# Performance work log

Measured on AMD Instinct MI355X. Metric: run time of the kernel, lower is better.

Reference implementation:

```python
import jax, jax.numpy as jnp
import numpy as np

D_MODEL = 512
H = 8
D_K = D_MODEL // H


def setup_inputs() -> dict:
    key = jax.random.key(0)
    ks = jax.random.split(key, 11)
    B, S = 2, 2048
    scale = 1.0 / np.sqrt(D_MODEL)
    return {
        "q": jax.random.normal(ks[0], (B, S, D_MODEL), jnp.float32),
        "v": jax.random.normal(ks[1], (B, S, D_MODEL), jnp.float32),
        "k": jax.random.normal(ks[2], (B, S, D_MODEL), jnp.float32),
        "w_q": jax.random.normal(ks[3], (D_MODEL, D_MODEL), jnp.float32) * scale,
        "b_q": jnp.zeros((D_MODEL,), jnp.float32),
        "w_k": jax.random.normal(ks[4], (D_MODEL, D_MODEL), jnp.float32) * scale,
        "b_k": jnp.zeros((D_MODEL,), jnp.float32),
        "w_v": jax.random.normal(ks[5], (D_MODEL, D_MODEL), jnp.float32) * scale,
        "b_v": jnp.zeros((D_MODEL,), jnp.float32),
        "w_o": jax.random.normal(ks[6], (D_MODEL, D_MODEL), jnp.float32) * scale,
        "b_o": jnp.zeros((D_MODEL,), jnp.float32),
    }


def reference(q, v, k, w_q, b_q, w_k, b_k, w_v, b_v, w_o, b_o):
    B, S, _ = q.shape
    # projections (nn.Linear: x @ W.T + b)
    query = q @ w_q.T + b_q
    key_t = k @ w_k.T + b_k
    value = v @ w_v.T + b_v
    # split heads: [B, S, H, D_K] -> [B, H, S, D_K]
    query = query.reshape(B, S, H, D_K).transpose(0, 2, 1, 3)
    key_t = key_t.reshape(B, S, H, D_K).transpose(0, 2, 1, 3)
    value = value.reshape(B, S, H, D_K).transpose(0, 2, 1, 3)
    # unfused attention: full [B, H, S, S] score matrix
    scores = jnp.einsum("bhqd,bhkd->bhqk", query, key_t) / jnp.sqrt(
        jnp.asarray(D_K, query.dtype)
    )
    attn = jax.nn.softmax(scores, axis=-1)  # dropout inactive in eval
    x = jnp.einsum("bhqk,bhkd->bhqd", attn, value)
    # merge heads and output projection
    x = x.transpose(0, 2, 1, 3).reshape(B, S, D_MODEL)
    return x @ w_o.T + b_o
```

## Files before the change

kernel.cpp:

```cpp
#include <hip/hip_runtime.h>
#include <hip/hip_bf16.h>


typedef __attribute__((ext_vector_type(8))) short short8;
typedef __attribute__((ext_vector_type(4))) short short4v;
typedef __attribute__((ext_vector_type(4))) float f32x4;
typedef __attribute__((ext_vector_type(4))) unsigned int uint4v;

#define DM 512
#define SEQ 2048
#define NROW 4096
#define LOG2E 1.44269504088896341f
#define MFMA(a, b, c) __builtin_amdgcn_mfma_f32_16x16x32_bf16(a, b, c, 0, 0, 0)
#define FENCE() __asm__ __volatile__("" ::: "memory")

#if __has_builtin(__builtin_amdgcn_exp2f)
#define EXP2(x) __builtin_amdgcn_exp2f(x)
#else
#define EXP2(x) exp2f(x)
#endif

__device__ __forceinline__ float bf_bits2f(short s) {
    unsigned int u = ((unsigned int)(unsigned short)s) << 16;
    return __builtin_bit_cast(float, u);
}
__device__ __forceinline__ short f2bf_r(float f) {
    unsigned int u = __builtin_bit_cast(unsigned int, f) + 0x8000u;
    return (short)(u >> 16);
}
__device__ __forceinline__ unsigned int pack_bf16(float lo, float hi) {
    unsigned int ul = __builtin_bit_cast(unsigned int, lo) + 0x8000u;
    unsigned int uh = __builtin_bit_cast(unsigned int, hi) + 0x8000u;
    return __builtin_amdgcn_perm(uh, ul, 0x07060302u);
}

__device__ __forceinline__ void gload_lds16(const void* src, void* lds_dst) {
    __builtin_amdgcn_global_load_lds(
        (const __attribute__((address_space(1))) unsigned int*)src,
        (__attribute__((address_space(3))) unsigned int*)lds_dst, 16, 0, 0);
}

template <int ROWS, int NW, int SH = 0>
__device__ __forceinline__ void stage_tile(const short* __restrict__ gsrc, size_t gstride,
                                           short* lds, int wave, int lane) {
    constexpr int ISSUES = ROWS * 8 / (64 * NW);
    #pragma unroll
    for (int i = 0; i < ISSUES; i++) {
        const int blk = i * NW + wave;
        const int g = blk * 64 + lane;
        const int row = g >> 3;
        const int cb = (g & 7) ^ ((row >> SH) & 7);
        gload_lds16(gsrc + (size_t)row * gstride + cb * 8, lds + (size_t)blk * 512);
    }
}

__device__ __forceinline__ bool detect_f32(const unsigned int* __restrict__ q, int* cnt_lds) {
    if (threadIdx.x == 0) *cnt_lds = 0;
    __syncthreads();
    int local = 0;
    for (int i = threadIdx.x; i < 1024; i += blockDim.x) {
        unsigned int lo = q[i] & 0x7FFFu;
        if (lo >= 0x3000u && lo < 0x4400u) local++;
    }
    if (local) atomicAdd(cnt_lds, local);
    __syncthreads();
    return *cnt_lds < 512;
}

struct ConvArgs { const void* src[11]; short* dst[11]; int n[11]; int* flag; };
__global__ void convert_all(ConvArgs a) {
    __shared__ int cnt;
    const bool f32m = detect_f32((const unsigned int*)a.src[0], &cnt);
    if (threadIdx.x == 0) *a.flag = f32m ? 1 : 0;
    const int tid = blockIdx.x * 256 + threadIdx.x;
    const int stride = gridDim.x * 256;
    if (f32m) {
        for (int s = 0; s < 11; s++) {
            const float4* sp = (const float4*)a.src[s];
            short4v* dp = (short4v*)a.dst[s];
            const int n4 = a.n[s] >> 2;
            for (int i = tid; i < n4; i += stride) {
                float4 v = sp[i];
                short4v o;
                o[0] = f2bf_r(v.x); o[1] = f2bf_r(v.y);
                o[2] = f2bf_r(v.z); o[3] = f2bf_r(v.w);
                dp[i] = o;
            }
        }
    } else {
        for (int s = 0; s < 11; s++) {
            const short4v* sp = (const short4v*)a.src[s];
            short4v* dp = (short4v*)a.dst[s];
            const int n4 = a.n[s] >> 2;
            for (int i = tid; i < n4; i += stride) dp[i] = sp[i];
        }
    }
}

template <int MT, int NT>
__device__ __forceinline__ void gemm_core(const short* __restrict__ A,
                                          const short* __restrict__ W,
                                          int m0, int n0, short* Alds, short* Blds,
                                          int wave, int lane,
                                          f32x4 (&acc)[MT / 64][NT / 16]) {
    const int rc = lane & 15, quad = lane >> 4;
    const short* Ag = A + (size_t)m0 * DM;
    const short* Bg = W + (size_t)n0 * DM;
    constexpr int ABUF = MT * 64, BBUF = NT * 64;
    constexpr int INFLIGHT = (MT + NT) * 8 / 256;
    constexpr int NITER = DM / 64;

    stage_tile<MT, 4>(Ag, DM, Alds, wave, lane);
    stage_tile<NT, 4>(Bg, DM, Blds, wave, lane);

    for (int i = 0; i < NITER; i++) {
        const int cur = i & 1;
        const short* Ac = Alds + cur * ABUF;
        const short* Bc = Blds + cur * BBUF;
        if (i + 1 < NITER) {
            stage_tile<MT, 4>(Ag + (i + 1) * 64, DM, Alds + (cur ^ 1) * ABUF, wave, lane);
            stage_tile<NT, 4>(Bg + (i + 1) * 64, DM, Blds + (cur ^ 1) * BBUF, wave, lane);
            __builtin_amdgcn_s_waitcnt(0x3F70 | INFLIGHT);
        } else {
            __builtin_amdgcn_s_waitcnt(0x3F70);
        }
        FENCE();
        __builtin_amdgcn_s_barrier();
        FENCE();
        #pragma unroll
        for (int h = 0; h < 2; h++) {
            short8 bf[NT / 16];
            #pragma unroll
            for (int nt = 0; nt < NT / 16; nt++) {
                const int br = nt * 16 + rc;
                bf[nt] = *(const short8*)&Bc[br * 64 + (((quad + 4 * h) ^ (br & 7)) * 8)];
            }
            #pragma unroll
            for (int ms = 0; ms < MT / 64; ms++) {
                const int ar = wave * (MT / 4) + ms * 16 + rc;
                short8 af = *(const short8*)&Ac[ar * 64 + (((quad + 4 * h) ^ (ar & 7)) * 8)];
                #pragma unroll
                for (int nt = 0; nt < NT / 16; nt++)
                    acc[ms][nt] = MFMA(af, bf[nt], acc[ms][nt]);
            }
        }
        FENCE();
        __builtin_amdgcn_s_barrier();
        FENCE();
    }
}

struct QKVArgs {
    const short* A[3]; const short* W[3]; const short* Bi[3];
    short* Cq; short* Ck; short* Cv;
};
__global__ __launch_bounds__(256, 2) void qkv_gemm(QKVArgs args) {
    __shared__ __align__(16) short Alds[2][128 * 64];
    __shared__ __align__(16) short Blds[2][128 * 64];
    const int z = blockIdx.z;
    const int wave = threadIdx.x >> 6, lane = threadIdx.x & 63;
    const int rc = lane & 15, quad = lane >> 4;
    const int m0 = blockIdx.x * 128, n0 = blockIdx.y * 128;

    f32x4 acc[2][8] = {};
    gemm_core<128, 128>(args.A[z], args.W[z], m0, n0, &Alds[0][0], &Blds[0][0], wave, lane, acc);
    const short* bias = args.Bi[z];

    if (z == 2) {
        #pragma unroll
        for (int ms = 0; ms < 2; ms++) {
            const int mw = m0 + wave * 32 + ms * 16;
            const int b = mw >> 11, sb = (mw & 2047) + quad * 4;
            #pragma unroll
            for (int nt = 0; nt < 8; nt++) {
                const int dg = n0 + nt * 16 + rc;
                const int hh = dg >> 6, dd = dg & 63;
                const float bv = bf_bits2f(bias[dg]);
                short4v pk;
                #pragma unroll
                for (int r = 0; r < 4; r++) pk[r] = f2bf_r(acc[ms][nt][r] + bv);
                *(short4v*)(args.Cv + ((size_t)((b * 8 + hh) * 64 + dd)) * SEQ + sb) = pk;
            }
        }
    } else {
        short* C = (z == 0) ? args.Cq : args.Ck;
        const float sc = (z == 0) ? (0.125f * LOG2E) : 1.0f;
        #pragma unroll
        for (int ms = 0; ms < 2; ms++) {
            const int mw = m0 + wave * 32 + ms * 16;
            #pragma unroll
            for (int nt = 0; nt < 8; nt++) {
                const int col = n0 + nt * 16 + rc;
                const float bv = bf_bits2f(bias[col]);
                #pragma unroll
                for (int r = 0; r < 4; r++)
                    C[(size_t)(mw + quad * 4 + r) * DM + col] = f2bf_r((acc[ms][nt][r] + bv) * sc);
            }
        }
    }
}

__global__ __launch_bounds__(256, 4) void out_gemm(
    const short* __restrict__ A, const short* __restrict__ W,
    const short* __restrict__ bias, void* __restrict__ Cout,
    const int* __restrict__ dtf) {
    __shared__ __align__(16) short Alds[2][64 * 64];
    __shared__ __align__(16) short Blds[2][64 * 64];
    const bool f32out = (*dtf != 0);
    const int wave = threadIdx.x >> 6, lane = threadIdx.x & 63;
    const int rc = lane & 15, quad = lane >> 4;
    const int m0 = blockIdx.x * 64, n0 = blockIdx.y * 64;
    f32x4 acc[1][4] = {};
    gemm_core<64, 64>(A, W, m0, n0, &Alds[0][0], &Blds[0][0], wave, lane, acc);
    const int mw = m0 + wave * 16;
    #pragma unroll
    for (int nt = 0; nt < 4; nt++) {
        const int col = n0 + nt * 16 + rc;
        const float bv = bf_bits2f(bias[col]);
        #pragma unroll
        for (int r = 0; r < 4; r++) {
            const size_t idx = (size_t)(mw + quad * 4 + r) * DM + col;
            const float val = acc[0][nt][r] + bv;
            if (f32out) ((float*)Cout)[idx] = val;
            else        ((short*)Cout)[idx] = f2bf_r(val);
        }
    }
}

__global__ __launch_bounds__(512, 4) void attn_kernel(
    const short* __restrict__ Q, const short* __restrict__ K,
    const short* __restrict__ Vt, short* __restrict__ X)
{
    __shared__ __align__(16) short S[2][16384];

    const int wave = threadIdx.x >> 6, lane = threadIdx.x & 63;
    const int rc = lane & 15, quad = lane >> 4;
    const int qh = wave & 1, kh = wave >> 1;
    const int L = blockIdx.x;
    const int bh = (L & 7) * 2 + ((L >> 3) >> 5);
    const int qb = (L >> 3) & 31;
    const size_t baseQK = (size_t)(bh >> 3) * SEQ * DM + (size_t)(bh & 7) * 64;
    const short* Qb = Q + baseQK;
    const short* Kb = K + baseQK;
    const short* Vb = Vt + (size_t)bh * 64 * SEQ;
    const int q0 = qb * 64 + qh * 32;

    short8 qa[2][2];
    #pragma unroll
    for (int ms = 0; ms < 2; ms++)
        #pragma unroll
        for (int h = 0; h < 2; h++)
            qa[ms][h] = *(const short8*)(Qb + (size_t)(q0 + ms * 16 + rc) * DM + h * 32 + quad * 8);

    short8 ones;
    #pragma unroll
    for (int j = 0; j < 8; j++) ones[j] = (short)0x3F80;

    f32x4 o[4][2] = {};
    f32x4 lsum[2] = {};

    int koff[2][2], voff[4];
    #pragma unroll
    for (int kt = 0; kt < 2; kt++) {
        const int row = kh * 32 + rc * 2 + kt;
        #pragma unroll
        for (int h = 0; h < 2; h++)
            koff[kt][h] = row * 64 + (((quad + 4 * h) ^ ((row >> 1) & 7)) * 8);
    }
    #pragma unroll
    for (int dt = 0; dt < 4; dt++) {
        const int row = dt * 16 + rc;
        voff[dt] = row * 64 + ((((kh & 1) * 4 + quad) ^ (row & 7)) * 8);
    }

    stage_tile<128, 8, 1>(Kb, DM, &S[0][0], wave, lane);
    stage_tile<64, 8>(Vb, SEQ, &S[0][8192], wave, lane);
    stage_tile<64, 8>(Vb + 64, SEQ, &S[0][12288], wave, lane);
    __syncthreads();

    for (int it = 0; it < 16; ++it) {
        const int cur = it & 1;
        if (it + 1 < 16) {
            const int k0n = (it + 1) * 128;
            stage_tile<128, 8, 1>(Kb + (size_t)k0n * DM, DM, &S[cur ^ 1][0], wave, lane);
            stage_tile<64, 8>(Vb + k0n, SEQ, &S[cur ^ 1][8192], wave, lane);
            stage_tile<64, 8>(Vb + k0n + 64, SEQ, &S[cur ^ 1][12288], wave, lane);
        }

        const short* Kt = &S[cur][0];
        const short* Vl = &S[cur][8192 + (kh >> 1) * 4096];

        short8 kf[2][2];
        #pragma unroll
        for (int kt = 0; kt < 2; kt++)
            #pragma unroll
            for (int h = 0; h < 2; h++)
                kf[kt][h] = *(const short8*)&Kt[koff[kt][h]];
        f32x4 s[2][2];
        __builtin_amdgcn_s_setprio(1);
        #pragma unroll
        for (int ms = 0; ms < 2; ms++)
            #pragma unroll
            for (int kt = 0; kt < 2; kt++) {
                f32x4 t = {};
                t = MFMA(kf[kt][0], qa[ms][0], t);
                t = MFMA(kf[kt][1], qa[ms][1], t);
                s[ms][kt] = t;
            }
        __builtin_amdgcn_s_setprio(0);
        short8 pa[2];
        #pragma unroll
        for (int ms = 0; ms < 2; ms++) {
            uint4v w;
            #pragma unroll
            for (int r = 0; r < 4; r++)
                w[r] = pack_bf16(EXP2(s[ms][0][r]), EXP2(s[ms][1][r]));
            pa[ms] = __builtin_bit_cast(short8, w);
        }
        __builtin_amdgcn_s_setprio(1);
        #pragma unroll
        for (int ms = 0; ms < 2; ms++)
            lsum[ms] = MFMA(ones, pa[ms], lsum[ms]);
        #pragma unroll
        for (int dt = 0; dt < 4; dt++) {
            short8 v = *(const short8*)&Vl[voff[dt]];
            #pragma unroll
            for (int ms = 0; ms < 2; ms++)
                o[dt][ms] = MFMA(v, pa[ms], o[dt][ms]);
        }
        __builtin_amdgcn_s_setprio(0);
        __syncthreads();
    }

    float* OM = (float*)&S[0][0];
    float* LM = OM + 12288;
    if (kh > 0) {
        #pragma unroll
        for (int dt = 0; dt < 4; dt++)
            #pragma unroll
            for (int ms = 0; ms < 2; ms++) {
                const int e = (kh - 1) * 16 + (dt * 2 + ms) * 2 + qh;
                *(f32x4*)&OM[(e * 64 + lane) * 4] = o[dt][ms];
            }
        #pragma unroll
        for (int ms = 0; ms < 2; ms++)
            LM[((kh - 1) * 4 + qh * 2 + ms) * 64 + lane] = lsum[ms][0];
    }
    __syncthreads();
    if (kh == 0) {
        short* Xr = X + baseQK;
        #pragma unroll
        for (int ms = 0; ms < 2; ms++) {
            float l = lsum[ms][0];
            #pragma unroll
            for (int p = 0; p < 3; p++) l += LM[(p * 4 + qh * 2 + ms) * 64 + lane];
            const float inv = 1.0f / l;
            const size_t rowoff = (size_t)(q0 + ms * 16 + rc) * DM;
            #pragma unroll
            for (int dt = 0; dt < 4; dt++) {
                f32x4 acc = o[dt][ms];
                #pragma unroll
                for (int p = 0; p < 3; p++) {
                    const int e = p * 16 + (dt * 2 + ms) * 2 + qh;
                    const f32x4 op = *(const f32x4*)&OM[(e * 64 + lane) * 4];
                    #pragma unroll
                    for (int r = 0; r < 4; r++) acc[r] += op[r];
                }
                short4v pk;
                #pragma unroll
                for (int r = 0; r < 4; r++) pk[r] = f2bf_r(acc[r] * inv);
                *(short4v*)(Xr + rowoff + dt * 16 + quad * 4) = pk;
            }
        }
    }
}

extern "C" void kernel_launch(void* const* d_in, const int* in_sizes, int n_in,
                              void* d_out, int out_size, void* d_ws, size_t ws_size,
                              hipStream_t stream) {
    char* ws = (char*)d_ws;
    const size_t SEQB = (size_t)NROW * DM * sizeof(short);
    const size_t WB   = (size_t)DM * DM * sizeof(short);
    const size_t BB   = (size_t)DM * sizeof(short);

    size_t off = 0;
    short* qc = (short*)(ws + off); off += SEQB;
    short* vc = (short*)(ws + off); off += SEQB;
    short* kc = (short*)(ws + off); off += SEQB;
    short* wq = (short*)(ws + off); off += WB;
    short* wk = (short*)(ws + off); off += WB;
    short* wv = (short*)(ws + off); off += WB;
    short* wo = (short*)(ws + off); off += WB;
    short* bq = (short*)(ws + off); off += BB;
    short* bk = (short*)(ws + off); off += BB;
    short* bv = (short*)(ws + off); off += BB;
    short* bo = (short*)(ws + off); off += BB;
    off = (off + 255) & ~(size_t)255;
    short* Qp  = (short*)(ws + off); off += SEQB;
    short* Kp  = (short*)(ws + off); off += SEQB;
    short* Vtp = (short*)(ws + off); off += SEQB;
    short* Xp  = (short*)(ws + off); off += SEQB;
    int*   dtf = (int*)(ws + off);  off += 256;

    ConvArgs ca;
    const void* srcs[11] = {d_in[0], d_in[1], d_in[2], d_in[3], d_in[5], d_in[7],
                            d_in[9], d_in[4], d_in[6], d_in[8], d_in[10]};
    short* dsts[11] = {qc, vc, kc, wq, wk, wv, wo, bq, bk, bv, bo};
    int ns[11] = {NROW * DM, NROW * DM, NROW * DM, DM * DM, DM * DM, DM * DM,
                  DM * DM, DM, DM, DM, DM};
    for (int i = 0; i < 11; i++) { ca.src[i] = srcs[i]; ca.dst[i] = dsts[i]; ca.n[i] = ns[i]; }
    ca.flag = dtf;
    convert_all<<<1024, 256, 0, stream>>>(ca);

    QKVArgs qa;
    qa.A[0] = qc; qa.A[1] = kc; qa.A[2] = vc;
    qa.W[0] = wq; qa.W[1] = wk; qa.W[2] = wv;
    qa.Bi[0] = bq; qa.Bi[1] = bk; qa.Bi[2] = bv;
    qa.Cq = Qp; qa.Ck = Kp; qa.Cv = Vtp;
    qkv_gemm<<<dim3(NROW / 128, DM / 128, 3), 256, 0, stream>>>(qa);

    attn_kernel<<<dim3(512), 512, 0, stream>>>(Qp, Kp, Vtp, Xp);

    out_gemm<<<dim3(NROW / 64, DM / 64), 256, 0, stream>>>(
        Xp, wo, bo, d_out, dtf);
}
```

Measured before the change: 140.8 us.

## Fuse fp32-to-bf16 activation conversion into QKV GEMM A-tile loads

Drops the separate conversion of the q/k/v activations to bf16 and their bf16 copies in the workspace. The QKV GEMM now reads raw fp32 (or bf16) inputs into registers, packs them to bf16 and writes them into swizzled LDS, double-buffered against the MFMA loop. The convert kernel now handles only weights and biases and runs with fewer blocks. This saves a full read and write pass over the activations, but the A tile now goes through register-staged loads instead of direct global-to-LDS loads, and each A tile is re-read and re-converted by all four column blocks.

```diff
diff --git a/kernel.cpp b/kernel.cpp
--- a/kernel.cpp
+++ b/kernel.cpp
@@ -67,15 +67,16 @@
     return *cnt_lds < 512;
 }
 
-struct ConvArgs { const void* src[11]; short* dst[11]; int n[11]; int* flag; };
+struct ConvArgs { const void* detect_src; const void* src[8]; short* dst[8];
+                  int n[8]; int* flag; };
 __global__ void convert_all(ConvArgs a) {
     __shared__ int cnt;
-    const bool f32m = detect_f32((const unsigned int*)a.src[0], &cnt);
+    const bool f32m = detect_f32((const unsigned int*)a.detect_src, &cnt);
     if (threadIdx.x == 0) *a.flag = f32m ? 1 : 0;
     const int tid = blockIdx.x * 256 + threadIdx.x;
     const int stride = gridDim.x * 256;
     if (f32m) {
-        for (int s = 0; s < 11; s++) {
+        for (int s = 0; s < 8; s++) {
             const float4* sp = (const float4*)a.src[s];
             short4v* dp = (short4v*)a.dst[s];
             const int n4 = a.n[s] >> 2;
@@ -88,7 +89,7 @@
             }
         }
     } else {
-        for (int s = 0; s < 11; s++) {
+        for (int s = 0; s < 8; s++) {
             const short4v* sp = (const short4v*)a.src[s];
             short4v* dp = (short4v*)a.dst[s];
             const int n4 = a.n[s] >> 2;
@@ -97,75 +98,86 @@
     }
 }
 
-template <int MT, int NT>
-__device__ __forceinline__ void gemm_core(const short* __restrict__ A,
-                                          const short* __restrict__ W,
-                                          int m0, int n0, short* Alds, short* Blds,
-                                          int wave, int lane,
-                                          f32x4 (&acc)[MT / 64][NT / 16]) {
-    const int rc = lane & 15, quad = lane >> 4;
-    const short* Ag = A + (size_t)m0 * DM;
-    const short* Bg = W + (size_t)n0 * DM;
-    constexpr int ABUF = MT * 64, BBUF = NT * 64;
-    constexpr int INFLIGHT = (MT + NT) * 8 / 256;
-    constexpr int NITER = DM / 64;
-
-    stage_tile<MT, 4>(Ag, DM, Alds, wave, lane);
-    stage_tile<NT, 4>(Bg, DM, Blds, wave, lane);
-
-    for (int i = 0; i < NITER; i++) {
-        const int cur = i & 1;
-        const short* Ac = Alds + cur * ABUF;
-        const short* Bc = Blds + cur * BBUF;
-        if (i + 1 < NITER) {
-            stage_tile<MT, 4>(Ag + (i + 1) * 64, DM, Alds + (cur ^ 1) * ABUF, wave, lane);
-            stage_tile<NT, 4>(Bg + (i + 1) * 64, DM, Blds + (cur ^ 1) * BBUF, wave, lane);
-            __builtin_amdgcn_s_waitcnt(0x3F70 | INFLIGHT);
-        } else {
-            __builtin_amdgcn_s_waitcnt(0x3F70);
-        }
-        FENCE();
-        __builtin_amdgcn_s_barrier();
-        FENCE();
-        #pragma unroll
-        for (int h = 0; h < 2; h++) {
-            short8 bf[NT / 16];
-            #pragma unroll
-            for (int nt = 0; nt < NT / 16; nt++) {
-                const int br = nt * 16 + rc;
-                bf[nt] = *(const short8*)&Bc[br * 64 + (((quad + 4 * h) ^ (br & 7)) * 8)];
-            }
-            #pragma unroll
-            for (int ms = 0; ms < MT / 64; ms++) {
-                const int ar = wave * (MT / 4) + ms * 16 + rc;
-                short8 af = *(const short8*)&Ac[ar * 64 + (((quad + 4 * h) ^ (ar & 7)) * 8)];
-                #pragma unroll
-                for (int nt = 0; nt < NT / 16; nt++)
-                    acc[ms][nt] = MFMA(af, bf[nt], acc[ms][nt]);
-            }
-        }
-        FENCE();
-        __builtin_amdgcn_s_barrier();
-        FENCE();
-    }
-}
-
 struct QKVArgs {
-    const short* A[3]; const short* W[3]; const short* Bi[3];
+    const void* Araw[3];
+    const short* W[3]; const short* Bi[3];
     short* Cq; short* Ck; short* Cv;
+    const int* flag;
 };
 __global__ __launch_bounds__(256, 2) void qkv_gemm(QKVArgs args) {
     __shared__ __align__(16) short Alds[2][128 * 64];
     __shared__ __align__(16) short Blds[2][128 * 64];
     const int z = blockIdx.z;
+    const bool f32m = (*args.flag != 0);
     const int wave = threadIdx.x >> 6, lane = threadIdx.x & 63;
     const int rc = lane & 15, quad = lane >> 4;
     const int m0 = blockIdx.x * 128, n0 = blockIdx.y * 128;
+    const short* Bg = args.W[z] + (size_t)n0 * DM;
+
+    short8 areg[4];
+    auto loadA = [&](int kcol) {
+        #pragma unroll
+        for (int i = 0; i < 4; i++) {
+            const int g = (i * 4 + wave) * 64 + lane;
+            const int row = g >> 3;
+            const int cb = (g & 7) ^ (row & 7);
+            const size_t off = (size_t)(m0 + row) * DM + kcol + cb * 8;
+            if (f32m) {
+                const float* p = (const float*)args.Araw[z] + off;
+                const float4 x = *(const float4*)p;
+                const float4 y = *(const float4*)(p + 4);
+                uint4v w;
+                w[0] = pack_bf16(x.x, x.y); w[1] = pack_bf16(x.z, x.w);
+                w[2] = pack_bf16(y.x, y.y); w[3] = pack_bf16(y.z, y.w);
+                areg[i] = __builtin_bit_cast(short8, w);
+            } else {
+                areg[i] = *(const short8*)((const short*)args.Araw[z] + off);
+            }
+        }
+    };
+    auto writeA = [&](short* Ab) {
+        #pragma unroll
+        for (int i = 0; i < 4; i++)
+            *(short8*)(Ab + (size_t)(i * 4 + wave) * 512 + lane * 8) = areg[i];
+    };
 
     f32x4 acc[2][8] = {};
-    gemm_core<128, 128>(args.A[z], args.W[z], m0, n0, &Alds[0][0], &Blds[0][0], wave, lane, acc);
+
+    loadA(0);
+    stage_tile<128, 4>(Bg, DM, &Blds[0][0], wave, lane);
+    writeA(&Alds[0][0]);
+    __syncthreads();
+
+    for (int i = 0; i < 8; i++) {
+        const int cur = i & 1;
+        if (i + 1 < 8) {
+            loadA((i + 1) * 64);
+            stage_tile<128, 4>(Bg + (i + 1) * 64, DM, &Blds[cur ^ 1][0], wave, lane);
+        }
+        const short* Ac = &Alds[cur][0];
+        const short* Bc = &Blds[cur][0];
+        #pragma unroll
+        for (int h = 0; h < 2; h++) {
+            short8 bf[8];
+            #pragma unroll
+            for (int nt = 0; nt < 8; nt++) {
+                const int br = nt * 16 + rc;
+                bf[nt] = *(const short8*)&Bc[br * 64 + (((quad + 4 * h) ^ (br & 7)) * 8)];
+            }
+            #pragma unroll
+            for (int ms = 0; ms < 2; ms++) {
+                const int ar = wave * 32 + ms * 16 + rc;
+                short8 af = *(const short8*)&Ac[ar * 64 + (((quad + 4 * h) ^ (ar & 7)) * 8)];
+                #pragma unroll
+                for (int nt = 0; nt < 8; nt++)
+                    acc[ms][nt] = MFMA(af, bf[nt], acc[ms][nt]);
+            }
+        }
+        if (i + 1 < 8) writeA(&Alds[cur ^ 1][0]);
+        __syncthreads();
+    }
+
     const short* bias = args.Bi[z];
-
     if (z == 2) {
         #pragma unroll
         for (int ms = 0; ms < 2; ms++) {
@@ -210,8 +222,44 @@
     const int wave = threadIdx.x >> 6, lane = threadIdx.x & 63;
     const int rc = lane & 15, quad = lane >> 4;
     const int m0 = blockIdx.x * 64, n0 = blockIdx.y * 64;
-    f32x4 acc[1][4] = {};
-    gemm_core<64, 64>(A, W, m0, n0, &Alds[0][0], &Blds[0][0], wave, lane, acc);
+    const short* Ag = A + (size_t)m0 * DM;
+    const short* Bg = W + (size_t)n0 * DM;
+    f32x4 acc[4] = {};
+
+    stage_tile<64, 4>(Ag, DM, &Alds[0][0], wave, lane);
+    stage_tile<64, 4>(Bg, DM, &Blds[0][0], wave, lane);
+    for (int i = 0; i < 8; i++) {
+        const int cur = i & 1;
+        const short* Ac = &Alds[cur][0];
+        const short* Bc = &Blds[cur][0];
+        if (i + 1 < 8) {
+            stage_tile<64, 4>(Ag + (i + 1) * 64, DM, &Alds[cur ^ 1][0], wave, lane);
+            stage_tile<64, 4>(Bg + (i + 1) * 64, DM, &Blds[cur ^ 1][0], wave, lane);
+            __builtin_amdgcn_s_waitcnt(0x3F70 | 4);
+        } else {
+            __builtin_amdgcn_s_waitcnt(0x3F70);
+        }
+        FENCE();
+        __builtin_amdgcn_s_barrier();
+        FENCE();
+        #pragma unroll
+        for (int h = 0; h < 2; h++) {
+            short8 bf[4];
+            #pragma unroll
+            for (int nt = 0; nt < 4; nt++) {
+                const int br = nt * 16 + rc;
+                bf[nt] = *(const short8*)&Bc[br * 64 + (((quad + 4 * h) ^ (br & 7)) * 8)];
+            }
+            const int ar = wave * 16 + rc;
+            short8 af = *(const short8*)&Ac[ar * 64 + (((quad + 4 * h) ^ (ar & 7)) * 8)];
+            #pragma unroll
+            for (int nt = 0; nt < 4; nt++)
+                acc[nt] = MFMA(af, bf[nt], acc[nt]);
+        }
+        FENCE();
+        __builtin_amdgcn_s_barrier();
+        FENCE();
+    }
     const int mw = m0 + wave * 16;
     #pragma unroll
     for (int nt = 0; nt < 4; nt++) {
@@ -220,7 +268,7 @@
         #pragma unroll
         for (int r = 0; r < 4; r++) {
             const size_t idx = (size_t)(mw + quad * 4 + r) * DM + col;
-            const float val = acc[0][nt][r] + bv;
+            const float val = acc[nt][r] + bv;
             if (f32out) ((float*)Cout)[idx] = val;
             else        ((short*)Cout)[idx] = f2bf_r(val);
         }
@@ -384,9 +432,6 @@
     const size_t BB   = (size_t)DM * sizeof(short);
 
     size_t off = 0;
-    short* qc = (short*)(ws + off); off += SEQB;
-    short* vc = (short*)(ws + off); off += SEQB;
-    short* kc = (short*)(ws + off); off += SEQB;
     short* wq = (short*)(ws + off); off += WB;
     short* wk = (short*)(ws + off); off += WB;
     short* wv = (short*)(ws + off); off += WB;
@@ -403,20 +448,23 @@
     int*   dtf = (int*)(ws + off);  off += 256;
 
     ConvArgs ca;
-    const void* srcs[11] = {d_in[0], d_in[1], d_in[2], d_in[3], d_in[5], d_in[7],
-                            d_in[9], d_in[4], d_in[6], d_in[8], d_in[10]};
-    short* dsts[11] = {qc, vc, kc, wq, wk, wv, wo, bq, bk, bv, bo};
-    int ns[11] = {NROW * DM, NROW * DM, NROW * DM, DM * DM, DM * DM, DM * DM,
-                  DM * DM, DM, DM, DM, DM};
-    for (int i = 0; i < 11; i++) { ca.src[i] = srcs[i]; ca.dst[i] = dsts[i]; ca.n[i] = ns[i]; }
+    ca.detect_src = d_in[0];
+    const void* srcs[8] = {d_in[3], d_in[5], d_in[7], d_in[9],
+                           d_in[4], d_in[6], d_in[8], d_in[10]};
+    short* dsts[8] = {wq, wk, wv, wo, bq, bk, bv, bo};
+    int ns[8] = {DM * DM, DM * DM, DM * DM, DM * DM, DM, DM, DM, DM};
+    for (int i = 0; i < 8; i++) { ca.src[i] = srcs[i]; ca.dst[i] = dsts[i]; ca.n[i] = ns[i]; }
     ca.flag = dtf;
-    convert_all<<<1024, 256, 0, stream>>>(ca);
+    convert_all<<<256, 256, 0, stream>>>(ca);
 
     QKVArgs qa;
-    qa.A[0] = qc; qa.A[1] = kc; qa.A[2] = vc;
+    qa.Araw[0] = d_in[0];
+    qa.Araw[1] = d_in[2];
+    qa.Araw[2] = d_in[1];
     qa.W[0] = wq; qa.W[1] = wk; qa.W[2] = wv;
     qa.Bi[0] = bq; qa.Bi[1] = bk; qa.Bi[2] = bv;
     qa.Cq = Qp; qa.Ck = Kp; qa.Cv = Vtp;
+    qa.flag = dtf;
     qkv_gemm<<<dim3(NROW / 128, DM / 128, 3), 256, 0, stream>>>(qa);
 
     attn_kernel<<<dim3(512), 512, 0, stream>>>(Qp, Kp, Vtp, Xp);
```

Measured after the change: 144.9 us. 1.03x slower.
